# Kernel optimization log

Hardware: AMD Instinct MI355X
Metric: run time of the kernel (lower is better)

## Reference

```python
import jax, jax.numpy as jnp
import numpy as np

COS_EPS = 1e-8    # torch.nn.CosineSimilarity default eps
NORM_EPS = 1e-12  # torch F.normalize default eps


def _cosine_gram(x, y):
    # Pairwise cosine similarity as a GEMM over row-normalized vectors,
    # matching torch: dot / max(|x|*|y|, eps). Avoids O(b^2*d) broadcast.
    dots = x @ y.T                               # [b, b]
    nx = jnp.linalg.norm(x, axis=1)              # [b]
    ny = jnp.linalg.norm(y, axis=1)              # [b]
    return dots / jnp.maximum(nx[:, None] * ny[None, :], COS_EPS)


def _row_normalize(g):
    # torch F.normalize(p=2, dim=1): x / max(||x||, eps)
    n = jnp.linalg.norm(g, axis=1, keepdims=True)
    return g / jnp.maximum(n, NORM_EPS)


def setup_inputs() -> dict:
    key = jax.random.key(0)
    k1, k2, k3, k4 = jax.random.split(key, 4)
    bsz, dim = 8192, 128
    return {
        "zxs": jax.random.normal(k1, (bsz, dim), dtype=jnp.float32),
        "zys": jax.random.normal(k2, (bsz, dim), dtype=jnp.float32),
        "zxt": jax.random.normal(k3, (bsz, dim), dtype=jnp.float32),
        "zyt": jax.random.normal(k4, (bsz, dim), dtype=jnp.float32),
        "temperature": jnp.asarray(0.5, dtype=jnp.float32),
    }


def reference(zxs, zys, zxt, zyt, temperature):
    bsz = zxs.shape[0]
    sim_s = _row_normalize(_cosine_gram(zxs, zys) / temperature)  # [b, b]
    sim_t = _row_normalize(_cosine_gram(zxt, zyt) / temperature)  # [b, b]
    g_diff = sim_t - sim_s
    loss = jnp.sum(g_diff * g_diff) / (bsz * bsz)
    return loss
```

## Files before the change

kernel.cpp:

```cpp
#include <hip/hip_runtime.h>
#include <hip/hip_bf16.h>


typedef __attribute__((ext_vector_type(8))) short short8;
typedef __attribute__((ext_vector_type(4))) float float4v;

#define BSZ 8192
#define DIM 128
#define NP  64
#define INV_B2 1.4901161193847656e-08f

__device__ __forceinline__ short f2bf(float x) {
    union { __hip_bfloat16 b; short s; } u;
    u.b = __float2bfloat16(x);
    return u.s;
}

__global__ __launch_bounds__(256) void prep(
    const float* __restrict__ Yt, const float* __restrict__ Ys,
    short* __restrict__ YT, float* __restrict__ out)
{
    __shared__ float rsum[2][32];
    __shared__ float invn[32];

    const int tid   = threadIdx.x;
    const int lane  = tid & 63;
    const int wave  = tid >> 6;
    const int d     = tid & 127;
    const int khalf = tid >> 7;
    const int chunk = blockIdx.x;
    const int mat   = blockIdx.y;
    const float* Y  = mat ? Ys : Yt;

    if (chunk == 0 && mat == 0 && tid == 0) out[0] = 0.f;

    float v[16];
    const float* base = Y + (size_t)(chunk * 32 + khalf * 16) * DIM + d;
    #pragma unroll
    for (int i = 0; i < 16; ++i) v[i] = base[(size_t)i * DIM];

    #pragma unroll
    for (int i = 0; i < 16; ++i) {
        float ss = v[i] * v[i];
        #pragma unroll
        for (int off = 1; off < 64; off <<= 1) ss += __shfl_xor(ss, off);
        if (lane == 0) rsum[wave & 1][khalf * 16 + i] = ss;
    }
    __syncthreads();
    if (tid < 32) {
        float s = rsum[0][tid] + rsum[1][tid];
        invn[tid] = (s > 0.f) ? rsqrtf(s) : 0.f;
    }
    __syncthreads();

    short* yt = YT + ((size_t)mat * 128 + d) * BSZ + chunk * 32 + khalf * 16;
    #pragma unroll
    for (int g = 0; g < 2; ++g) {
        short8 pk;
        #pragma unroll
        for (int j = 0; j < 8; ++j) {
            int i = g * 8 + j;
            pk[j] = f2bf(v[i] * invn[khalf * 16 + i]);
        }
        *(short8*)&yt[g * 8] = pk;
    }
}

__global__ __launch_bounds__(512) void gram_g(
    const short* __restrict__ YT, float* __restrict__ partial)
{
    const int tid  = threadIdx.x;
    const int lane = tid & 63;
    const int s1   = tid >> 6;
    const int q    = lane >> 4;
    const int l15  = lane & 15;
    const int split = blockIdx.x;
    const int gram  = blockIdx.y;

    const short* Ta = (gram == 1) ? YT + (size_t)128 * BSZ : YT;
    const short* Tb = (gram == 0) ? YT : YT + (size_t)128 * BSZ;
    const int k0 = split * 128;

    float4v acc[8];
    #pragma unroll
    for (int s2 = 0; s2 < 8; ++s2) acc[s2] = (float4v){0.f, 0.f, 0.f, 0.f};

    #pragma unroll
    for (int kk = 0; kk < 4; ++kk) {
        const int ko = k0 + kk * 32 + q * 8;
        short8 fa = *(const short8*)&Ta[(size_t)(s1 * 16 + l15) * BSZ + ko];
        short8 fb[8];
        #pragma unroll
        for (int s2 = 0; s2 < 8; ++s2)
            fb[s2] = *(const short8*)&Tb[(size_t)(s2 * 16 + l15) * BSZ + ko];
        #pragma unroll
        for (int s2 = 0; s2 < 8; ++s2)
            acc[s2] = __builtin_amdgcn_mfma_f32_16x16x32_bf16(fa, fb[s2], acc[s2], 0, 0, 0);
    }

    float* P = partial + ((size_t)(gram * NP + split) << 14);
    #pragma unroll
    for (int s2 = 0; s2 < 8; ++s2)
        #pragma unroll
        for (int r = 0; r < 4; ++r)
            P[((s1 * 16 + q * 4 + r) << 7) + s2 * 16 + l15] = acc[s2][r];
}

__global__ __launch_bounds__(256) void reduce_g(
    const float* __restrict__ partial, __hip_bfloat16* __restrict__ Gb)
{
    int o = blockIdx.x * 256 + threadIdx.x;
    int g = o >> 14, rem = o & 16383;
    float s = 0.f;
    for (int b = 0; b < NP; ++b)
        s += partial[((size_t)(g * NP + b) << 14) + rem];
    int d1 = rem >> 7, d2 = rem & 127;
    Gb[(g << 14) + (d2 << 7) + d1] = __float2bfloat16(s);
}

__global__ __launch_bounds__(256) void quad_k(
    const float* __restrict__ Xt, const float* __restrict__ Xs,
    const __hip_bfloat16* __restrict__ Gb, float* __restrict__ out)
{
    const int tid  = threadIdx.x;
    const int lane = tid & 63;
    const int wave = tid >> 6;
    const int q    = lane >> 4;
    const int l15  = lane & 15;
    const int g    = wave & 1;
    const int h    = wave >> 1;
    const int rbase = blockIdx.x * 32 + g * 16;

    short8 At[4], As[4];
    #pragma unroll
    for (int kk = 0; kk < 4; ++kk) {
        const float* pt = Xt + (size_t)(rbase + l15) * DIM + kk * 32 + q * 8;
        const float* ps = Xs + (size_t)(rbase + l15) * DIM + kk * 32 + q * 8;
        float4 t0 = *(const float4*)pt, t1 = *(const float4*)(pt + 4);
        float4 s0 = *(const float4*)ps, s1 = *(const float4*)(ps + 4);
        short8 a, b;
        a[0]=f2bf(t0.x); a[1]=f2bf(t0.y); a[2]=f2bf(t0.z); a[3]=f2bf(t0.w);
        a[4]=f2bf(t1.x); a[5]=f2bf(t1.y); a[6]=f2bf(t1.z); a[7]=f2bf(t1.w);
        b[0]=f2bf(s0.x); b[1]=f2bf(s0.y); b[2]=f2bf(s0.z); b[3]=f2bf(s0.w);
        b[4]=f2bf(s1.x); b[5]=f2bf(s1.y); b[6]=f2bf(s1.z); b[7]=f2bf(s1.w);
        At[kk] = a; As[kk] = b;
    }

    float fA[4] = {0,0,0,0}, fB[4] = {0,0,0,0}, fC[4] = {0,0,0,0};
    const short* G = (const short*)Gb;

    #pragma unroll
    for (int nti = 0; nti < 4; ++nti) {
        int d2 = (h * 4 + nti) * 16 + l15;
        float4v qt = {0.f,0.f,0.f,0.f}, qs = qt, qc = qt;
        #pragma unroll
        for (int kk = 0; kk < 4; ++kk) {
            int off = (d2 << 7) + kk * 32 + q * 8;
            short8 Bt = *(const short8*)&G[off];
            short8 Bs = *(const short8*)&G[16384 + off];
            short8 Bm = *(const short8*)&G[32768 + off];
            qt = __builtin_amdgcn_mfma_f32_16x16x32_bf16(At[kk], Bt, qt, 0, 0, 0);
            qs = __builtin_amdgcn_mfma_f32_16x16x32_bf16(As[kk], Bs, qs, 0, 0, 0);
            qc = __builtin_amdgcn_mfma_f32_16x16x32_bf16(At[kk], Bm, qc, 0, 0, 0);
        }
        #pragma unroll
        for (int r = 0; r < 4; ++r) {
            int row = rbase + q * 4 + r;
            float xtv = Xt[(size_t)row * DIM + d2];
            float xsv = Xs[(size_t)row * DIM + d2];
            fA[r] += qt[r] * xtv;
            fB[r] += qs[r] * xsv;
            fC[r] += qc[r] * xsv;
        }
    }

    __shared__ float cmb[2][16][8];
    #pragma unroll
    for (int r = 0; r < 4; ++r) {
        float A = fA[r], B = fB[r], C = fC[r];
        #pragma unroll
        for (int off = 1; off < 16; off <<= 1) {
            A += __shfl_xor(A, off);
            B += __shfl_xor(B, off);
            C += __shfl_xor(C, off);
        }
        if (l15 == 0) {
            cmb[g][q * 4 + r][h * 4 + 0] = A;
            cmb[g][q * 4 + r][h * 4 + 1] = B;
            cmb[g][q * 4 + r][h * 4 + 2] = C;
        }
    }
    __syncthreads();

    if (wave == 0) {
        float wl = 0.f;
        if (tid < 32) {
            int gg = tid >> 4, row = tid & 15;
            float A = cmb[gg][row][0] + cmb[gg][row][4];
            float B = cmb[gg][row][1] + cmb[gg][row][5];
            float C = cmb[gg][row][2] + cmb[gg][row][6];
            wl = 2.f - 2.f * C * rsqrtf(A * B);
        }
        #pragma unroll
        for (int off = 1; off < 64; off <<= 1) wl += __shfl_xor(wl, off);
        if (tid == 0) atomicAdd(out, wl * INV_B2);
    }
}

extern "C" void kernel_launch(void* const* d_in, const int* in_sizes, int n_in,
                              void* d_out, int out_size, void* d_ws, size_t ws_size,
                              hipStream_t stream) {
    const float* zxs = (const float*)d_in[0];
    const float* zys = (const float*)d_in[1];
    const float* zxt = (const float*)d_in[2];
    const float* zyt = (const float*)d_in[3];
    float* out = (float*)d_out;

    char* ws = (char*)d_ws;
    short* YT = (short*)ws;
    float* partial = (float*)(ws + (size_t)4 * 1024 * 1024);
    __hip_bfloat16* Gb = (__hip_bfloat16*)(ws + (size_t)4 * 1024 * 1024
                                              + (size_t)3 * NP * 16384 * sizeof(float));

    prep    <<<dim3(256, 2), 256, 0, stream>>>(zyt, zys, YT, out);
    gram_g  <<<dim3(NP, 3),  512, 0, stream>>>(YT, partial);
    reduce_g<<<192,          256, 0, stream>>>(partial, Gb);
    quad_k  <<<256,          256, 0, stream>>>(zxt, zxs, Gb, out);
}
```

Before: 103.4 us.

## Fuse four pipeline kernels into one cooperative kernel with grid syncs

Merges the prep, gram, reduce and quadratic-form stages into a single cooperative kernel of 256 blocks × 512 threads, with grid.sync between stages. Each stage is remapped to 512-thread blocks: prep handles four row groups per block and quad splits the column tiles across four wave pairs. The aim is to remove three kernel launch boundaries and their drain/ramp gaps. The cost is grid-wide barrier overhead and idle blocks in the smaller stages, with a fallback to four separate launches if the cooperative launch fails.

```diff
diff --git a/kernel.cpp b/kernel.cpp
--- a/kernel.cpp
+++ b/kernel.cpp
@@ -1,6 +1,9 @@
 #include <hip/hip_runtime.h>
 #include <hip/hip_bf16.h>
-
+#include <hip/hip_cooperative_groups.h>
+
+
+namespace cg = cooperative_groups;
 
 typedef __attribute__((ext_vector_type(8))) short short8;
 typedef __attribute__((ext_vector_type(4))) float float4v;
@@ -16,26 +19,24 @@
     return u.s;
 }
 
-__global__ __launch_bounds__(256) void prep(
+__device__ __forceinline__ void do_prep(
+    int bid, int tid,
     const float* __restrict__ Yt, const float* __restrict__ Ys,
     short* __restrict__ YT, float* __restrict__ out)
 {
-    __shared__ float rsum[2][32];
-    __shared__ float invn[32];
-
-    const int tid   = threadIdx.x;
-    const int lane  = tid & 63;
-    const int wave  = tid >> 6;
-    const int d     = tid & 127;
-    const int khalf = tid >> 7;
-    const int chunk = blockIdx.x;
-    const int mat   = blockIdx.y;
-    const float* Y  = mat ? Ys : Yt;
-
-    if (chunk == 0 && mat == 0 && tid == 0) out[0] = 0.f;
+    __shared__ float rsum[8][16];
+    __shared__ float invn[4][16];
+
+    const int lane = tid & 63, wave = tid >> 6;
+    const int slot = tid >> 7, d = tid & 127;
+    const int u = bid * 4 + slot;
+    const int mat = u >> 9, rg = u & 511;
+    const float* Y = mat ? Ys : Yt;
+
+    if (bid == 0 && tid == 0) out[0] = 0.f;
 
     float v[16];
-    const float* base = Y + (size_t)(chunk * 32 + khalf * 16) * DIM + d;
+    const float* base = Y + (size_t)(rg * 16) * DIM + d;
     #pragma unroll
     for (int i = 0; i < 16; ++i) v[i] = base[(size_t)i * DIM];
 
@@ -44,38 +45,39 @@
         float ss = v[i] * v[i];
         #pragma unroll
         for (int off = 1; off < 64; off <<= 1) ss += __shfl_xor(ss, off);
-        if (lane == 0) rsum[wave & 1][khalf * 16 + i] = ss;
+        if (lane == 0) rsum[wave][i] = ss;
     }
     __syncthreads();
-    if (tid < 32) {
-        float s = rsum[0][tid] + rsum[1][tid];
-        invn[tid] = (s > 0.f) ? rsqrtf(s) : 0.f;
+    if (tid < 64) {
+        int s = tid >> 4, i = tid & 15;
+        float sum = rsum[2 * s][i] + rsum[2 * s + 1][i];
+        invn[s][i] = (sum > 0.f) ? rsqrtf(sum) : 0.f;
     }
     __syncthreads();
 
-    short* yt = YT + ((size_t)mat * 128 + d) * BSZ + chunk * 32 + khalf * 16;
+    short* yt = YT + ((size_t)mat * 128 + d) * BSZ + rg * 16;
     #pragma unroll
     for (int g = 0; g < 2; ++g) {
         short8 pk;
         #pragma unroll
         for (int j = 0; j < 8; ++j) {
             int i = g * 8 + j;
-            pk[j] = f2bf(v[i] * invn[khalf * 16 + i]);
+            pk[j] = f2bf(v[i] * invn[slot][i]);
         }
         *(short8*)&yt[g * 8] = pk;
     }
 }
 
-__global__ __launch_bounds__(512) void gram_g(
+__device__ __forceinline__ void do_gram(
+    int bid, int tid,
     const short* __restrict__ YT, float* __restrict__ partial)
 {
-    const int tid  = threadIdx.x;
     const int lane = tid & 63;
     const int s1   = tid >> 6;
     const int q    = lane >> 4;
     const int l15  = lane & 15;
-    const int split = blockIdx.x;
-    const int gram  = blockIdx.y;
+    const int gram  = bid >> 6;
+    const int split = bid & 63;
 
     const short* Ta = (gram == 1) ? YT + (size_t)128 * BSZ : YT;
     const short* Tb = (gram == 0) ? YT : YT + (size_t)128 * BSZ;
@@ -106,30 +108,33 @@
             P[((s1 * 16 + q * 4 + r) << 7) + s2 * 16 + l15] = acc[s2][r];
 }
 
-__global__ __launch_bounds__(256) void reduce_g(
+__device__ __forceinline__ void do_reduce(
+    int bid, int tid,
     const float* __restrict__ partial, __hip_bfloat16* __restrict__ Gb)
 {
-    int o = blockIdx.x * 256 + threadIdx.x;
-    int g = o >> 14, rem = o & 16383;
+    const int o = bid * 512 + tid;
+    const int g = o >> 14, rem = o & 16383;
     float s = 0.f;
+    #pragma unroll
     for (int b = 0; b < NP; ++b)
         s += partial[((size_t)(g * NP + b) << 14) + rem];
-    int d1 = rem >> 7, d2 = rem & 127;
-    Gb[(g << 14) + (d2 << 7) + d1] = __float2bfloat16(s);
-}
-
-__global__ __launch_bounds__(256) void quad_k(
+    Gb[(g << 14) + ((rem & 127) << 7) + (rem >> 7)] = __float2bfloat16(s);
+}
+
+__device__ __forceinline__ void do_quad(
+    int bid, int tid,
     const float* __restrict__ Xt, const float* __restrict__ Xs,
     const __hip_bfloat16* __restrict__ Gb, float* __restrict__ out)
 {
-    const int tid  = threadIdx.x;
+    __shared__ float cmb[2][16][4][3];
+
     const int lane = tid & 63;
     const int wave = tid >> 6;
     const int q    = lane >> 4;
     const int l15  = lane & 15;
     const int g    = wave & 1;
-    const int h    = wave >> 1;
-    const int rbase = blockIdx.x * 32 + g * 16;
+    const int hq   = wave >> 1;
+    const int rbase = bid * 32 + g * 16;
 
     short8 At[4], As[4];
     #pragma unroll
@@ -150,8 +155,8 @@
     const short* G = (const short*)Gb;
 
     #pragma unroll
-    for (int nti = 0; nti < 4; ++nti) {
-        int d2 = (h * 4 + nti) * 16 + l15;
+    for (int nti = 0; nti < 2; ++nti) {
+        int d2 = (hq * 2 + nti) * 16 + l15;
         float4v qt = {0.f,0.f,0.f,0.f}, qs = qt, qc = qt;
         #pragma unroll
         for (int kk = 0; kk < 4; ++kk) {
@@ -174,7 +179,6 @@
         }
     }
 
-    __shared__ float cmb[2][16][8];
     #pragma unroll
     for (int r = 0; r < 4; ++r) {
         float A = fA[r], B = fB[r], C = fC[r];
@@ -185,9 +189,9 @@
             C += __shfl_xor(C, off);
         }
         if (l15 == 0) {
-            cmb[g][q * 4 + r][h * 4 + 0] = A;
-            cmb[g][q * 4 + r][h * 4 + 1] = B;
-            cmb[g][q * 4 + r][h * 4 + 2] = C;
+            cmb[g][q * 4 + r][hq][0] = A;
+            cmb[g][q * 4 + r][hq][1] = B;
+            cmb[g][q * 4 + r][hq][2] = C;
         }
     }
     __syncthreads();
@@ -196,9 +200,12 @@
         float wl = 0.f;
         if (tid < 32) {
             int gg = tid >> 4, row = tid & 15;
-            float A = cmb[gg][row][0] + cmb[gg][row][4];
-            float B = cmb[gg][row][1] + cmb[gg][row][5];
-            float C = cmb[gg][row][2] + cmb[gg][row][6];
+            float A = cmb[gg][row][0][0] + cmb[gg][row][1][0]
+                    + cmb[gg][row][2][0] + cmb[gg][row][3][0];
+            float B = cmb[gg][row][0][1] + cmb[gg][row][1][1]
+                    + cmb[gg][row][2][1] + cmb[gg][row][3][1];
+            float C = cmb[gg][row][0][2] + cmb[gg][row][1][2]
+                    + cmb[gg][row][2][2] + cmb[gg][row][3][2];
             wl = 2.f - 2.f * C * rsqrtf(A * B);
         }
         #pragma unroll
@@ -206,14 +213,50 @@
         if (tid == 0) atomicAdd(out, wl * INV_B2);
     }
 }
+
+__global__ __launch_bounds__(512) void fused(
+    const float* __restrict__ Xt, const float* __restrict__ Xs,
+    const float* __restrict__ Yt, const float* __restrict__ Ys,
+    short* __restrict__ YT, float* __restrict__ partial,
+    __hip_bfloat16* __restrict__ Gb, float* __restrict__ out)
+{
+    cg::grid_group grid = cg::this_grid();
+    const int bid = blockIdx.x, tid = threadIdx.x;
+
+    do_prep(bid, tid, Yt, Ys, YT, out);
+    grid.sync();
+    if (bid < 192) do_gram(bid, tid, YT, partial);
+    grid.sync();
+    if (bid < 96) do_reduce(bid, tid, partial, Gb);
+    grid.sync();
+    do_quad(bid, tid, Xt, Xs, Gb, out);
+}
+
+__global__ __launch_bounds__(512) void prep_k(
+    const float* __restrict__ Yt, const float* __restrict__ Ys,
+    short* __restrict__ YT, float* __restrict__ out)
+{ do_prep(blockIdx.x, threadIdx.x, Yt, Ys, YT, out); }
+
+__global__ __launch_bounds__(512) void gram_k(
+    const short* __restrict__ YT, float* __restrict__ partial)
+{ do_gram(blockIdx.x, threadIdx.x, YT, partial); }
+
+__global__ __launch_bounds__(512) void reduce_k(
+    const float* __restrict__ partial, __hip_bfloat16* __restrict__ Gb)
+{ do_reduce(blockIdx.x, threadIdx.x, partial, Gb); }
+
+__global__ __launch_bounds__(512) void quad_kk(
+    const float* __restrict__ Xt, const float* __restrict__ Xs,
+    const __hip_bfloat16* __restrict__ Gb, float* __restrict__ out)
+{ do_quad(blockIdx.x, threadIdx.x, Xt, Xs, Gb, out); }
 
 extern "C" void kernel_launch(void* const* d_in, const int* in_sizes, int n_in,
                               void* d_out, int out_size, void* d_ws, size_t ws_size,
                               hipStream_t stream) {
-    const float* zxs = (const float*)d_in[0];
-    const float* zys = (const float*)d_in[1];
-    const float* zxt = (const float*)d_in[2];
-    const float* zyt = (const float*)d_in[3];
+    const float* Xs = (const float*)d_in[0];
+    const float* Ys = (const float*)d_in[1];
+    const float* Xt = (const float*)d_in[2];
+    const float* Yt = (const float*)d_in[3];
     float* out = (float*)d_out;
 
     char* ws = (char*)d_ws;
@@ -222,8 +265,15 @@
     __hip_bfloat16* Gb = (__hip_bfloat16*)(ws + (size_t)4 * 1024 * 1024
                                               + (size_t)3 * NP * 16384 * sizeof(float));
 
-    prep    <<<dim3(256, 2), 256, 0, stream>>>(zyt, zys, YT, out);
-    gram_g  <<<dim3(NP, 3),  512, 0, stream>>>(YT, partial);
-    reduce_g<<<192,          256, 0, stream>>>(partial, Gb);
-    quad_k  <<<256,          256, 0, stream>>>(zxt, zxs, Gb, out);
-}
+    void* args[8] = { (void*)&Xt, (void*)&Xs, (void*)&Yt, (void*)&Ys,
+                      (void*)&YT, (void*)&partial, (void*)&Gb, (void*)&out };
+    hipError_t e = hipLaunchCooperativeKernel((const void*)fused, dim3(256),
+                                              dim3(512), args, 0, stream);
+    if (e != hipSuccess) {
+        (void)hipGetLastError();
+        prep_k  <<<256, 512, 0, stream>>>(Yt, Ys, YT, out);
+        gram_k  <<<192, 512, 0, stream>>>(YT, partial);
+        reduce_k<<< 96, 512, 0, stream>>>(partial, Gb);
+        quad_kk <<<256, 512, 0, stream>>>(Xt, Xs, Gb, out);
+    }
+}
```

After: 210.1 us. 103% more time.

## Replace split-K gram plus reduce kernel with direct output-tiled gram kernel

Applied to the files above, without the earlier changes.

The 128x128 Gram matrices used to be computed by split-K over 64 blocks per gram, which wrote fp32 partials to global memory, followed by a separate reduction kernel. Each block now owns one 16x16 output tile and loops over the full K=8192 across its 8 waves. The partial sums are reduced in shared memory and written straight to the bf16 G buffer. This drops one kernel launch and the partial-buffer traffic, at the cost of each block reading full K rows, which means more total reads of YT per tile and long serial MFMA chains per wave.

```diff
diff --git a/kernel.cpp b/kernel.cpp
--- a/kernel.cpp
+++ b/kernel.cpp
@@ -7,7 +7,6 @@
 
 #define BSZ 8192
 #define DIM 128
-#define NP  64
 #define INV_B2 1.4901161193847656e-08f
 
 __device__ __forceinline__ short f2bf(float x) {
@@ -66,56 +65,53 @@
     }
 }
 
-__global__ __launch_bounds__(512) void gram_g(
-    const short* __restrict__ YT, float* __restrict__ partial)
+__global__ __launch_bounds__(512) void gram_direct(
+    const short* __restrict__ YT, __hip_bfloat16* __restrict__ Gb)
 {
+    __shared__ float red[8][256];
+
     const int tid  = threadIdx.x;
     const int lane = tid & 63;
-    const int s1   = tid >> 6;
+    const int w    = tid >> 6;
     const int q    = lane >> 4;
     const int l15  = lane & 15;
-    const int split = blockIdx.x;
-    const int gram  = blockIdx.y;
+    const int gram = blockIdx.x >> 6;
+    const int t    = blockIdx.x & 63;
+    const int ti   = t >> 3, tj = t & 7;
 
     const short* Ta = (gram == 1) ? YT + (size_t)128 * BSZ : YT;
     const short* Tb = (gram == 0) ? YT : YT + (size_t)128 * BSZ;
-    const int k0 = split * 128;
-
-    float4v acc[8];
-    #pragma unroll
-    for (int s2 = 0; s2 < 8; ++s2) acc[s2] = (float4v){0.f, 0.f, 0.f, 0.f};
-
-    #pragma unroll
-    for (int kk = 0; kk < 4; ++kk) {
-        const int ko = k0 + kk * 32 + q * 8;
-        short8 fa = *(const short8*)&Ta[(size_t)(s1 * 16 + l15) * BSZ + ko];
-        short8 fb[8];
-        #pragma unroll
-        for (int s2 = 0; s2 < 8; ++s2)
-            fb[s2] = *(const short8*)&Tb[(size_t)(s2 * 16 + l15) * BSZ + ko];
-        #pragma unroll
-        for (int s2 = 0; s2 < 8; ++s2)
-            acc[s2] = __builtin_amdgcn_mfma_f32_16x16x32_bf16(fa, fb[s2], acc[s2], 0, 0, 0);
-    }
-
-    float* P = partial + ((size_t)(gram * NP + split) << 14);
-    #pragma unroll
-    for (int s2 = 0; s2 < 8; ++s2)
-        #pragma unroll
-        for (int r = 0; r < 4; ++r)
-            P[((s1 * 16 + q * 4 + r) << 7) + s2 * 16 + l15] = acc[s2][r];
-}
-
-__global__ __launch_bounds__(256) void reduce_g(
-    const float* __restrict__ partial, __hip_bfloat16* __restrict__ Gb)
-{
-    int o = blockIdx.x * 256 + threadIdx.x;
-    int g = o >> 14, rem = o & 16383;
-    float s = 0.f;
-    for (int b = 0; b < NP; ++b)
-        s += partial[((size_t)(g * NP + b) << 14) + rem];
-    int d1 = rem >> 7, d2 = rem & 127;
-    Gb[(g << 14) + (d2 << 7) + d1] = __float2bfloat16(s);
+
+    const short* pa = Ta + (size_t)(ti * 16 + l15) * BSZ + w * 1024 + q * 8;
+    const short* pb = Tb + (size_t)(tj * 16 + l15) * BSZ + w * 1024 + q * 8;
+
+    float4v acc[4];
+    #pragma unroll
+    for (int a = 0; a < 4; ++a) acc[a] = (float4v){0.f, 0.f, 0.f, 0.f};
+
+    #pragma unroll
+    for (int kk = 0; kk < 32; kk += 4) {
+        #pragma unroll
+        for (int a = 0; a < 4; ++a) {
+            short8 fa = *(const short8*)&pa[(kk + a) * 32];
+            short8 fb = *(const short8*)&pb[(kk + a) * 32];
+            acc[a] = __builtin_amdgcn_mfma_f32_16x16x32_bf16(fa, fb, acc[a], 0, 0, 0);
+        }
+    }
+
+    #pragma unroll
+    for (int r = 0; r < 4; ++r)
+        red[w][(q * 4 + r) * 16 + l15] = acc[0][r] + acc[1][r] + acc[2][r] + acc[3][r];
+    __syncthreads();
+
+    if (tid < 256) {
+        const int d1i = tid & 15, d2i = tid >> 4;
+        float s = 0.f;
+        #pragma unroll
+        for (int ww = 0; ww < 8; ++ww) s += red[ww][d1i * 16 + d2i];
+        Gb[((size_t)gram << 14) + ((tj * 16 + d2i) << 7) + ti * 16 + d1i]
+            = __float2bfloat16(s);
+    }
 }
 
 __global__ __launch_bounds__(256) void quad_k(
@@ -218,12 +214,9 @@
 
     char* ws = (char*)d_ws;
     short* YT = (short*)ws;
-    float* partial = (float*)(ws + (size_t)4 * 1024 * 1024);
-    __hip_bfloat16* Gb = (__hip_bfloat16*)(ws + (size_t)4 * 1024 * 1024
-                                              + (size_t)3 * NP * 16384 * sizeof(float));
-
-    prep    <<<dim3(256, 2), 256, 0, stream>>>(zyt, zys, YT, out);
-    gram_g  <<<dim3(NP, 3),  512, 0, stream>>>(YT, partial);
-    reduce_g<<<192,          256, 0, stream>>>(partial, Gb);
-    quad_k  <<<256,          256, 0, stream>>>(zxt, zxs, Gb, out);
-}
+    __hip_bfloat16* Gb = (__hip_bfloat16*)(ws + (size_t)4 * 1024 * 1024);
+
+    prep       <<<dim3(256, 2), 256, 0, stream>>>(zyt, zys, YT, out);
+    gram_direct<<<192,          512, 0, stream>>>(YT, Gb);
+    quad_k     <<<256,          256, 0, stream>>>(zxt, zxs, Gb, out);
+}
```

Measured after the change: 101.5 us. About the same (-1.9%).
